# Performance work log

Hardware: AMD Instinct MI355X
Metric: run time of the kernel (lower is better)

The kernel has to match this reference:

```python
import jax, jax.numpy as jnp
import numpy as np

B, Q, S, D, H = 4, 1024, 4096, 256, 8
HD = D // H
NEG = -1000000000.0


def setup_inputs() -> dict:
    key = jax.random.key(0)
    ks = jax.random.split(key, 12)
    s = 1.0 / np.sqrt(D)
    inp = {
        "query": jax.random.normal(ks[0], (B, Q, D), jnp.float32),
        "key": jax.random.normal(ks[1], (B, S, D), jnp.float32),
        "value": jax.random.normal(ks[2], (B, S, D), jnp.float32),
        "attention_mask": jax.random.randint(ks[3], (B, Q, S), 0, 2) > 0,
        # nn.Linear weights stored as [out, in]; we apply x @ W.T + b
        "wq": jax.random.uniform(ks[4], (D, D), jnp.float32, -s, s),
        "bq": jnp.zeros((D,), jnp.float32),
        "wk": jax.random.uniform(ks[5], (D, D), jnp.float32, -s, s),
        "bk": jnp.zeros((D,), jnp.float32),
        "wv": jax.random.uniform(ks[6], (D, D), jnp.float32, -s, s),
        "bv": jnp.zeros((D,), jnp.float32),
        "wo": jax.random.uniform(ks[7], (D, D), jnp.float32, -s, s),
        "bo": jnp.zeros((D,), jnp.float32),
        "ln_g": jnp.ones((D,), jnp.float32),
        "ln_b": jnp.zeros((D,), jnp.float32),
    }
    return inp


def _layernorm(x, g, b, eps=1e-5):
    mu = jnp.mean(x, axis=-1, keepdims=True)
    var = jnp.var(x, axis=-1, keepdims=True)
    return (x - mu) * jax.lax.rsqrt(var + eps) * g + b


def reference(query, key, value, attention_mask, wq, bq, wk, bk, wv, bv, wo, bo, ln_g, ln_b):
    residual = query
    x = _layernorm(query, ln_g, ln_b)
    q = x @ wq.T + bq                       # [B,Q,D]
    k = key @ wk.T + bk                     # [B,S,D]
    v = value @ wv.T + bv                   # [B,S,D]
    q = q.reshape(B, Q, H, HD).transpose(0, 2, 1, 3)   # [B,H,Q,HD]
    k = k.reshape(B, S, H, HD).transpose(0, 2, 1, 3)   # [B,H,S,HD]
    v = v.reshape(B, S, H, HD).transpose(0, 2, 1, 3)   # [B,H,S,HD]
    scale = HD ** -0.5
    scores = jnp.einsum("bhqd,bhsd->bhqs", q, k) * scale   # [B,H,Q,S]
    scores = jnp.where(attention_mask[:, None, :, :], scores, NEG)
    attn = jax.nn.softmax(scores, axis=-1)
    # dropout is identity in eval/inference mode
    out = jnp.einsum("bhqs,bhsd->bhqd", attn, v)            # [B,H,Q,HD]
    out = out.transpose(0, 2, 1, 3).reshape(B, Q, D)
    out = out @ wo.T + bo
    return out + residual
```

## Files before the change

### kernel.cpp

```cpp
#include <hip/hip_runtime.h>
#include <cmath>

#define BQ 4
#define QL 1024
#define SL 4096
#define DM 256
#define NH 8
#define HD 32
#define NROWS 32768
#define NSPLIT 4
#define SEG (SL / NSPLIT)

typedef __attribute__((ext_vector_type(8))) short short8;
typedef __attribute__((ext_vector_type(4))) short short4v;
typedef __attribute__((ext_vector_type(4))) float f32x4;
typedef __attribute__((ext_vector_type(4))) unsigned int uint4v;
typedef unsigned long long u64;

#define MFMA16(a, b, c) __builtin_amdgcn_mfma_f32_16x16x32_bf16((a), (b), (c), 0, 0, 0)

__device__ __forceinline__ short f2bf(float f) {
  union { float f; unsigned int u; } x; x.f = f;
  unsigned int r = x.u + 0x7FFFu + ((x.u >> 16) & 1u);
  return (short)(r >> 16);
}
__device__ __forceinline__ unsigned int fu(float f) {
  union { float f; unsigned int u; } x; x.f = f; return x.u;
}

__global__ __launch_bounds__(256) void wcvt_kernel(const float* __restrict__ wq,
                                                   const float* __restrict__ wk,
                                                   const float* __restrict__ wv,
                                                   const float* __restrict__ wo,
                                                   const uint4v* __restrict__ mask4,
                                                   unsigned int* __restrict__ flags,
                                                   short* __restrict__ w16) {
  if (blockIdx.x == 0) {
    __shared__ int fA, fB;
    if (threadIdx.x == 0) { fA = 0; fB = 0; }
    __syncthreads();
    unsigned int a = 0, bb = 0;
#pragma unroll
    for (int i = 0; i < 16; ++i) {
      uint4v v = mask4[threadIdx.x * 16 + i];
#pragma unroll
      for (int e = 0; e < 4; ++e) {
        a |= (v[e] & 0xFEFEFEFEu);
        bb |= (v[e] & 0xFFFFFF00u);
      }
    }
    if (a) atomicOr(&fA, 1);
    if (bb) atomicOr(&fB, 1);
    __syncthreads();
    if (threadIdx.x == 0) flags[0] = (fA || !fB) ? 4u : 1u;
  }
  const int i = blockIdx.x * 256 + threadIdx.x;
  const float* src;
  short* dst;
  if (i < 8192)       { src = wq + i * 8;            dst = w16 + i * 8; }
  else if (i < 16384) { src = wk + (i - 8192) * 8;   dst = w16 + 65536 + (i - 8192) * 8; }
  else if (i < 24576) { src = wv + (i - 16384) * 8;  dst = w16 + 131072 + (i - 16384) * 8; }
  else                { src = wo + (i - 24576) * 8;  dst = w16 + 196608 + (i - 24576) * 8; }
  f32x4 a0 = *(const f32x4*)src;
  f32x4 a1 = *(const f32x4*)(src + 4);
  short8 o;
#pragma unroll
  for (int e = 0; e < 4; ++e) { o[e] = f2bf(a0[e]); o[4 + e] = f2bf(a1[e]); }
  *(short8*)dst = o;
}

__global__ __launch_bounds__(256) void maskbits_kernel(const void* __restrict__ mask,
                                                       const unsigned int* __restrict__ flags,
                                                       u64* __restrict__ MB) {
  const int i = blockIdx.x * 256 + threadIdx.x;
  u64 bits = 0;
  if (flags[0] == 4u) {
    const uint4v* src = (const uint4v*)mask + (size_t)i * 16;
#pragma unroll
    for (int c = 0; c < 16; ++c) {
      uint4v v = src[c];
      unsigned int nib = 0;
#pragma unroll
      for (int e = 0; e < 4; ++e) nib |= (v[e] != 0u ? 1u : 0u) << e;
      bits |= (u64)nib << ((c & 3) * 16 + (c >> 2) * 4);
    }
  } else {
    const uint4v* src = (const uint4v*)mask + (size_t)i * 4;
#pragma unroll
    for (int c = 0; c < 4; ++c) {
      uint4v v = src[c];
#pragma unroll
      for (int e4 = 0; e4 < 4; ++e4) {
        const unsigned int u = v[e4];
        unsigned int nib = 0;
        nib |= (u & 0x000000FFu) ? 1u : 0u;
        nib |= (u & 0x0000FF00u) ? 2u : 0u;
        nib |= (u & 0x00FF0000u) ? 4u : 0u;
        nib |= (u & 0xFF000000u) ? 8u : 0u;
        bits |= (u64)nib << (e4 * 16 + c * 4);
      }
    }
  }
  MB[i] = bits;
}

__global__ __launch_bounds__(256) void ln_q_kernel(const float* __restrict__ x,
                                                   const float* __restrict__ gw,
                                                   const float* __restrict__ bw,
                                                   short* __restrict__ out) {
  const int lane = threadIdx.x & 63;
  const int row = blockIdx.x * 4 + (threadIdx.x >> 6);
  const float* xr = x + (size_t)row * DM;
  f32x4 v = *(const f32x4*)(xr + lane * 4);
  float s = v[0] + v[1] + v[2] + v[3];
  float s2 = v[0]*v[0] + v[1]*v[1] + v[2]*v[2] + v[3]*v[3];
#pragma unroll
  for (int m = 1; m < 64; m <<= 1) { s += __shfl_xor(s, m); s2 += __shfl_xor(s2, m); }
  const float mu = s * (1.0f / DM);
  const float var = s2 * (1.0f / DM) - mu * mu;
  const float inv = rsqrtf(var + 1e-5f);
  f32x4 gv = *(const f32x4*)(gw + lane * 4);
  f32x4 bv = *(const f32x4*)(bw + lane * 4);
  short4v o;
#pragma unroll
  for (int i = 0; i < 4; ++i) o[i] = f2bf((v[i] - mu) * inv * gv[i] + bv[i]);
  *(short4v*)(out + (size_t)row * DM + lane * 4) = o;
}

template <int AF32, int EPI>
__global__ __launch_bounds__(256) void gemm_bt(const void* __restrict__ Ap,
                                               const short* __restrict__ W16,
                                               const float* __restrict__ bias,
                                               void* __restrict__ outp,
                                               const float* __restrict__ resid,
                                               float oscale) {
  __shared__ __align__(16) short As[64][72];
  __shared__ __align__(16) short Bs[64][72];
  const int t = threadIdx.x;
  const int lane = t & 63, w = t >> 6;
  const int wm = w >> 1, wn = w & 1;
  const int g = lane >> 4, lr = lane & 15, gsh = g * 4;
  const int bid = blockIdx.x;
  const int x = bid & 7, j = bid >> 3;
  const int mt8 = gridDim.x >> 5;
  const int m0 = (x * mt8 + (j >> 2)) * 64;
  const int n0 = (j & 3) * 64;
  const int row = (t * 2) >> 3, cc0 = (t * 2) & 7;
  f32x4 acc[2][2] = {};

  const float* Af = (const float*)Ap;
  const short* A16 = (const short*)Ap;
  f32x4 apf[2][2];
  short8 aps[2];
  short8 bn[2];
#pragma unroll
  for (int c = 0; c < 2; ++c) {
    if (AF32) {
      const float* s = Af + (size_t)(m0 + row) * DM + (cc0 + c) * 8;
      apf[c][0] = *(const f32x4*)s;
      apf[c][1] = *(const f32x4*)(s + 4);
    } else {
      aps[c] = *(const short8*)(A16 + (size_t)(m0 + row) * DM + (cc0 + c) * 8);
    }
    bn[c] = *(const short8*)(W16 + (size_t)(n0 + row) * DM + (cc0 + c) * 8);
  }
  for (int k0 = 0; k0 < DM; k0 += 64) {
    if (k0) __syncthreads();
#pragma unroll
    for (int c = 0; c < 2; ++c) {
      short8 sv;
      if (AF32) {
#pragma unroll
        for (int e = 0; e < 4; ++e) { sv[e] = f2bf(apf[c][0][e]); sv[4 + e] = f2bf(apf[c][1][e]); }
      } else {
        sv = aps[c];
      }
      *(short8*)&As[row][(cc0 + c) * 8] = sv;
      *(short8*)&Bs[row][(cc0 + c) * 8] = bn[c];
    }
    __syncthreads();
    if (k0 < DM - 64) {
#pragma unroll
      for (int c = 0; c < 2; ++c) {
        if (AF32) {
          const float* s = Af + (size_t)(m0 + row) * DM + k0 + 64 + (cc0 + c) * 8;
          apf[c][0] = *(const f32x4*)s;
          apf[c][1] = *(const f32x4*)(s + 4);
        } else {
          aps[c] = *(const short8*)(A16 + (size_t)(m0 + row) * DM + k0 + 64 + (cc0 + c) * 8);
        }
        bn[c] = *(const short8*)(W16 + (size_t)(n0 + row) * DM + k0 + 64 + (cc0 + c) * 8);
      }
    }
#pragma unroll
    for (int ks = 0; ks < 2; ++ks) {
      short8 af[2], bfr[2];
#pragma unroll
      for (int i = 0; i < 2; ++i) af[i] = *(const short8*)&As[wm * 32 + i * 16 + lr][ks * 32 + g * 8];
#pragma unroll
      for (int jj = 0; jj < 2; ++jj) bfr[jj] = *(const short8*)&Bs[wn * 32 + jj * 16 + lr][ks * 32 + g * 8];
#pragma unroll
      for (int i = 0; i < 2; ++i)
#pragma unroll
        for (int jj = 0; jj < 2; ++jj) acc[i][jj] = MFMA16(af[i], bfr[jj], acc[i][jj]);
    }
  }
  if (EPI == 2) {
#pragma unroll
    for (int i = 0; i < 2; ++i)
#pragma unroll
      for (int jj = 0; jj < 2; ++jj)
#pragma unroll
        for (int r = 0; r < 4; ++r) {
          const int rr = m0 + wm * 32 + i * 16 + gsh + r;
          const int col = n0 + wn * 32 + jj * 16 + lr;
          ((float*)outp)[(size_t)rr * DM + col] =
              acc[i][jj][r] + bias[col] + resid[(size_t)rr * DM + col];
        }
  } else if (EPI == 0 || EPI == 1) {
    __syncthreads();
#pragma unroll
    for (int i = 0; i < 2; ++i)
#pragma unroll
      for (int jj = 0; jj < 2; ++jj) {
        const int nl = wn * 32 + jj * 16 + lr;
        const float bv = bias[n0 + nl];
#pragma unroll
        for (int r = 0; r < 4; ++r)
          As[wm * 32 + i * 16 + gsh + r][nl] = f2bf((acc[i][jj][r] + bv) * oscale);
      }
    __syncthreads();
#pragma unroll
    for (int c = 0; c < 2; ++c) {
      const int idx = t * 2 + c, dl = idx >> 3, ch = idx & 7;
      *(short8*)((short*)outp + (size_t)(m0 + dl) * DM + n0 + ch * 8) =
          *(const short8*)&As[dl][ch * 8];
    }
  } else {
    __syncthreads();
#pragma unroll
    for (int i = 0; i < 2; ++i)
#pragma unroll
      for (int jj = 0; jj < 2; ++jj) {
        const int nl = wn * 32 + jj * 16 + lr;
        const float bv = bias[n0 + nl];
        short4v pk4;
#pragma unroll
        for (int r = 0; r < 4; ++r) pk4[r] = f2bf(acc[i][jj][r] + bv);
        *(short4v*)&As[nl][wm * 32 + i * 16 + gsh] = pk4;
      }
    __syncthreads();
    const int bidx = m0 >> 12, sbase = m0 & (SL - 1);
#pragma unroll
    for (int c = 0; c < 2; ++c) {
      const int idx = t * 2 + c, dl = idx >> 3, ch = idx & 7;
      *(short8*)((short*)outp + ((size_t)bidx * DM + n0 + dl) * SL + sbase + ch * 8) =
          *(const short8*)&As[dl][ch * 8];
    }
  }
}

__global__ __launch_bounds__(256, 4) void attn_kernel(const short* __restrict__ qb,
                                                      const short* __restrict__ kb,
                                                      const short* __restrict__ vbT,
                                                      const unsigned short* __restrict__ MB,
                                                      float* __restrict__ Op,
                                                      float* __restrict__ Lp) {
  __shared__ __align__(16) short Ks[2][64][40];
  __shared__ __align__(16) short Vs[2][32][76];

  const int n_ = blockIdx.x;
  const int x_ = n_ & 7, j_ = n_ >> 3;
  const int grp = ((j_ >> 5) << 3) + x_;
  const int within = j_ & 31;
  const int q0 = (within & 7) * 128;
  const int split = within >> 3;
  const int h = grp & 7, b = grp >> 3;

  const int t = threadIdx.x;
  const int l = t & 63, w = t >> 6;
  const int g = l >> 4, lr = l & 15, gsh = g * 4;
  const int qbase = q0 + w * 32;
  const int srow = t >> 2, scc = t & 3;
  const int vd = t >> 3, vsc = t & 7;

  const short* Kp = kb + ((size_t)b * SL + split * SEG + srow) * DM + h * HD + scc * 8;
  const short* Vp = vbT + ((size_t)(b * NH + h) * HD + vd) * SL + split * SEG + vsc * 8;
  const unsigned short* MBp0 =
      MB + (((size_t)(b * QL) + qbase + lr) * 64 + split * (SEG / 64)) * 4 + g;
  const unsigned short* MBp1 = MBp0 + 16 * 64 * 4;

  const short8 qf0 =
      *(const short8*)(qb + ((size_t)(b * QL) + qbase + lr) * DM + h * HD + g * 8);
  const short8 qf1 =
      *(const short8*)(qb + ((size_t)(b * QL) + qbase + 16 + lr) * DM + h * HD + g * 8);

  const short ONE = (short)0x3F80;
  const short8 ONES = {ONE, ONE, ONE, ONE, ONE, ONE, ONE, ONE};
  f32x4 Ov0[2] = {}, Ov1[2] = {};
  f32x4 Ls0 = {0.f, 0.f, 0.f, 0.f}, Ls1 = {0.f, 0.f, 0.f, 0.f};

  short8 kreg[2], vreg[2];
  unsigned int mbA[2], mbB[2];
  kreg[0] = *(const short8*)Kp;
  vreg[0] = *(const short8*)Vp;
  mbA[0] = MBp0[0]; mbB[0] = MBp1[0];
  kreg[1] = *(const short8*)(Kp + (size_t)64 * DM);
  vreg[1] = *(const short8*)(Vp + 64);
  mbA[1] = MBp0[4]; mbB[1] = MBp1[4];

#pragma unroll 2
  for (int it = 0; it < SEG / 64; ++it) {
    const int buf = it & 1;
    *(short8*)&Ks[buf][srow][scc * 8] = kreg[buf];
    {
      short4v lo = {vreg[buf][0], vreg[buf][1], vreg[buf][2], vreg[buf][3]};
      short4v hi = {vreg[buf][4], vreg[buf][5], vreg[buf][6], vreg[buf][7]};
      *(short4v*)&Vs[buf][vd][vsc * 8] = lo;
      *(short4v*)&Vs[buf][vd][vsc * 8 + 4] = hi;
    }
    const unsigned int mb0 = mbA[buf], mb1 = mbB[buf];
    __syncthreads();
    if (it < SEG / 64 - 2) {
      kreg[buf] = *(const short8*)(Kp + (size_t)(it + 2) * 64 * DM);
      vreg[buf] = *(const short8*)(Vp + (it + 2) * 64);
      mbA[buf] = MBp0[(it + 2) * 4];
      mbB[buf] = MBp1[(it + 2) * 4];
    }

    const f32x4 z = {0.f, 0.f, 0.f, 0.f};
    f32x4 sc0[4], sc1[4];
#pragma unroll
    for (int f = 0; f < 4; ++f) {
      short8 kf = *(const short8*)&Ks[buf][f * 16 + lr][g * 8];
      sc0[f] = MFMA16(kf, qf0, z);
      sc1[f] = MFMA16(kf, qf1, z);
    }
#pragma unroll
    for (int ks = 0; ks < 2; ++ks) {
      unsigned int pk0[2][2], pk1[2][2];
#pragma unroll
      for (int fi = 0; fi < 2; ++fi) {
        const int f = 2 * ks + fi;
        unsigned int p0[4], p1[4];
#pragma unroll
        for (int r = 0; r < 4; ++r) {
          const unsigned int m0b = (unsigned int)(-(int)((mb0 >> (f * 4 + r)) & 1u));
          const unsigned int m1b = (unsigned int)(-(int)((mb1 >> (f * 4 + r)) & 1u));
          p0[r] = fu(__builtin_amdgcn_exp2f(sc0[f][r])) & m0b;
          p1[r] = fu(__builtin_amdgcn_exp2f(sc1[f][r])) & m1b;
        }
        pk0[fi][0] = __builtin_amdgcn_perm(p0[0], p0[1], 0x03020706u);
        pk0[fi][1] = __builtin_amdgcn_perm(p0[2], p0[3], 0x03020706u);
        pk1[fi][0] = __builtin_amdgcn_perm(p1[0], p1[1], 0x03020706u);
        pk1[fi][1] = __builtin_amdgcn_perm(p1[2], p1[3], 0x03020706u);
      }
      union { unsigned int u[4]; short8 v; } pa0, pa1;
      pa0.u[0] = pk0[0][0]; pa0.u[1] = pk0[0][1]; pa0.u[2] = pk0[1][0]; pa0.u[3] = pk0[1][1];
      pa1.u[0] = pk1[0][0]; pa1.u[1] = pk1[0][1]; pa1.u[2] = pk1[1][0]; pa1.u[3] = pk1[1][1];
      Ls0 = MFMA16(pa0.v, ONES, Ls0);
      Ls1 = MFMA16(pa1.v, ONES, Ls1);
#pragma unroll
      for (int n = 0; n < 2; ++n) {
        short4v va = *(const short4v*)&Vs[buf][n * 16 + lr][(2 * ks) * 16 + gsh];
        short4v vb2 = *(const short4v*)&Vs[buf][n * 16 + lr][(2 * ks + 1) * 16 + gsh];
        union { short4v h[2]; short8 v; } vf;
        vf.h[0] = va; vf.h[1] = vb2;
        Ov0[n] = MFMA16(pa0.v, vf.v, Ov0[n]);
        Ov1[n] = MFMA16(pa1.v, vf.v, Ov1[n]);
      }
    }
  }
  const int ridx = (b * NH + h) * QL + qbase;
  const size_t pb = (size_t)split * NROWS + ridx;
#pragma unroll
  for (int n = 0; n < 2; ++n)
#pragma unroll
    for (int r = 0; r < 4; ++r) {
      Op[(pb + gsh + r) * 32 + n * 16 + lr] = Ov0[n][r];
      Op[(pb + 16 + gsh + r) * 32 + n * 16 + lr] = Ov1[n][r];
    }
  if (lr == 0) {
#pragma unroll
    for (int r = 0; r < 4; ++r) {
      Lp[pb + gsh + r] = Ls0[r];
      Lp[pb + 16 + gsh + r] = Ls1[r];
    }
  }
}

__global__ __launch_bounds__(256) void combine_kernel(const float* __restrict__ Op,
                                                      const float* __restrict__ Lp,
                                                      short* __restrict__ ao) {
  const int tid = blockIdx.x * 256 + threadIdx.x;
  const int r = tid >> 3;
  const int dq = (tid & 7) * 4;
  float den = 0.0f;
  f32x4 acc = {0.f, 0.f, 0.f, 0.f};
#pragma unroll
  for (int i = 0; i < NSPLIT; ++i) {
    den += Lp[(size_t)i * NROWS + r];
    const f32x4 o = *(const f32x4*)(Op + ((size_t)i * NROWS + r) * 32 + dq);
#pragma unroll
    for (int e = 0; e < 4; ++e) acc[e] += o[e];
  }
  const float inv = __builtin_amdgcn_rcpf(den);
  const int b = r >> 13, h = (r >> 10) & 7, q = r & 1023;
  short4v o;
#pragma unroll
  for (int i = 0; i < 4; ++i) o[i] = f2bf(acc[i] * inv);
  *(short4v*)(ao + ((size_t)(b * QL + q)) * DM + h * HD + dq) = o;
}

extern "C" void kernel_launch(void* const* d_in, const int* in_sizes, int n_in,
                              void* d_out, int out_size, void* d_ws, size_t ws_size,
                              hipStream_t stream) {
  const float* query = (const float*)d_in[0];
  const float* key   = (const float*)d_in[1];
  const float* value = (const float*)d_in[2];
  const void*  mask  = d_in[3];
  const float* wq = (const float*)d_in[4];
  const float* bq = (const float*)d_in[5];
  const float* wk = (const float*)d_in[6];
  const float* bk = (const float*)d_in[7];
  const float* wv = (const float*)d_in[8];
  const float* bv = (const float*)d_in[9];
  const float* wo = (const float*)d_in[10];
  const float* bo = (const float*)d_in[11];
  const float* lng = (const float*)d_in[12];
  const float* lnb = (const float*)d_in[13];
  float* out = (float*)d_out;

  char* ws = (char*)d_ws;
  unsigned int* flags = (unsigned int*)ws;
  float* Lp  = (float*)(ws + (4u << 10));
  short* xln = (short*)(ws + (2u << 20));
  short* qb  = (short*)(ws + (4u << 20));
  short* kb  = (short*)(ws + (6u << 20));
  short* vbT = (short*)(ws + (14u << 20));
  u64*   mbt = (u64*)(ws + (22u << 20));
  short* w16 = (short*)(ws + (24u << 20));
  float* Op  = (float*)(ws + (25u << 20));
  short* ao  = (short*)(ws + (41u << 20));

  const float qscale = (float)(1.4426950408889634 / sqrt((double)HD));

  wcvt_kernel<<<128, 256, 0, stream>>>(wq, wk, wv, wo, (const uint4v*)mask, flags, w16);
  maskbits_kernel<<<1024, 256, 0, stream>>>(mask, flags, mbt);
  ln_q_kernel<<<(BQ * QL) / 4, 256, 0, stream>>>(query, lng, lnb, xln);
  gemm_bt<0, 0><<<(BQ * QL / 64) * 4, 256, 0, stream>>>(xln, w16, bq, qb, nullptr, qscale);
  gemm_bt<1, 1><<<(BQ * SL / 64) * 4, 256, 0, stream>>>(key, w16 + 65536, bk, kb, nullptr, 1.0f);
  gemm_bt<1, 3><<<(BQ * SL / 64) * 4, 256, 0, stream>>>(value, w16 + 131072, bv, vbT, nullptr, 1.0f);
  attn_kernel<<<1024, 256, 0, stream>>>(qb, kb, vbT, (const unsigned short*)mbt, Op, Lp);
  combine_kernel<<<1024, 256, 0, stream>>>(Op, Lp, ao);
  gemm_bt<0, 2><<<(BQ * QL / 64) * 4, 256, 0, stream>>>(ao, w16 + 196608, bo, out, query, 1.0f);
}
```

Baseline: 94.83 us.

## Halve attention query tile per block to double grid and occupancy

Each attention block now processes 64 query rows (16 per wave) instead of 128 (32 per wave), and the grid grows from 1024 to 2048 blocks with launch bounds raised to 8 blocks per CU. The aim is more waves in flight to hide memory and MFMA latency. In exchange, every K/V tile is loaded from global memory and staged through LDS twice as often, which lowers reuse per loaded byte.

After: 110.9 us. 16.9% more time.

```diff
diff --git a/kernel.cpp b/kernel.cpp
--- a/kernel.cpp
+++ b/kernel.cpp
@@ -260,7 +260,7 @@
   }
 }
 
-__global__ __launch_bounds__(256, 4) void attn_kernel(const short* __restrict__ qb,
+__global__ __launch_bounds__(256, 8) void attn_kernel(const short* __restrict__ qb,
                                                       const short* __restrict__ kb,
                                                       const short* __restrict__ vbT,
                                                       const unsigned short* __restrict__ MB,
@@ -271,43 +271,40 @@
 
   const int n_ = blockIdx.x;
   const int x_ = n_ & 7, j_ = n_ >> 3;
-  const int grp = ((j_ >> 5) << 3) + x_;
-  const int within = j_ & 31;
-  const int q0 = (within & 7) * 128;
-  const int split = within >> 3;
+  const int grp = ((j_ >> 6) << 3) + x_;
+  const int within = j_ & 63;
+  const int q0 = (within & 15) * 64;
+  const int split = within >> 4;
   const int h = grp & 7, b = grp >> 3;
 
   const int t = threadIdx.x;
   const int l = t & 63, w = t >> 6;
   const int g = l >> 4, lr = l & 15, gsh = g * 4;
-  const int qbase = q0 + w * 32;
+  const int qbase = q0 + w * 16;
   const int srow = t >> 2, scc = t & 3;
   const int vd = t >> 3, vsc = t & 7;
 
   const short* Kp = kb + ((size_t)b * SL + split * SEG + srow) * DM + h * HD + scc * 8;
   const short* Vp = vbT + ((size_t)(b * NH + h) * HD + vd) * SL + split * SEG + vsc * 8;
-  const unsigned short* MBp0 =
+  const unsigned short* MBp =
       MB + (((size_t)(b * QL) + qbase + lr) * 64 + split * (SEG / 64)) * 4 + g;
-  const unsigned short* MBp1 = MBp0 + 16 * 64 * 4;
-
-  const short8 qf0 =
+
+  const short8 qf =
       *(const short8*)(qb + ((size_t)(b * QL) + qbase + lr) * DM + h * HD + g * 8);
-  const short8 qf1 =
-      *(const short8*)(qb + ((size_t)(b * QL) + qbase + 16 + lr) * DM + h * HD + g * 8);
 
   const short ONE = (short)0x3F80;
   const short8 ONES = {ONE, ONE, ONE, ONE, ONE, ONE, ONE, ONE};
-  f32x4 Ov0[2] = {}, Ov1[2] = {};
-  f32x4 Ls0 = {0.f, 0.f, 0.f, 0.f}, Ls1 = {0.f, 0.f, 0.f, 0.f};
+  f32x4 Ov[2] = {};
+  f32x4 Ls = {0.f, 0.f, 0.f, 0.f};
 
   short8 kreg[2], vreg[2];
-  unsigned int mbA[2], mbB[2];
+  unsigned int mbA[2];
   kreg[0] = *(const short8*)Kp;
   vreg[0] = *(const short8*)Vp;
-  mbA[0] = MBp0[0]; mbB[0] = MBp1[0];
+  mbA[0] = MBp[0];
   kreg[1] = *(const short8*)(Kp + (size_t)64 * DM);
   vreg[1] = *(const short8*)(Vp + 64);
-  mbA[1] = MBp0[4]; mbB[1] = MBp1[4];
+  mbA[1] = MBp[4];
 
 #pragma unroll 2
   for (int it = 0; it < SEG / 64; ++it) {
@@ -319,55 +316,46 @@
       *(short4v*)&Vs[buf][vd][vsc * 8] = lo;
       *(short4v*)&Vs[buf][vd][vsc * 8 + 4] = hi;
     }
-    const unsigned int mb0 = mbA[buf], mb1 = mbB[buf];
+    const unsigned int mb = mbA[buf];
     __syncthreads();
     if (it < SEG / 64 - 2) {
       kreg[buf] = *(const short8*)(Kp + (size_t)(it + 2) * 64 * DM);
       vreg[buf] = *(const short8*)(Vp + (it + 2) * 64);
-      mbA[buf] = MBp0[(it + 2) * 4];
-      mbB[buf] = MBp1[(it + 2) * 4];
+      mbA[buf] = MBp[(it + 2) * 4];
     }
 
     const f32x4 z = {0.f, 0.f, 0.f, 0.f};
-    f32x4 sc0[4], sc1[4];
+    f32x4 sc[4];
 #pragma unroll
     for (int f = 0; f < 4; ++f) {
       short8 kf = *(const short8*)&Ks[buf][f * 16 + lr][g * 8];
-      sc0[f] = MFMA16(kf, qf0, z);
-      sc1[f] = MFMA16(kf, qf1, z);
+      sc[f] = MFMA16(kf, qf, z);
     }
 #pragma unroll
     for (int ks = 0; ks < 2; ++ks) {
-      unsigned int pk0[2][2], pk1[2][2];
+      unsigned int pk[2][2];
 #pragma unroll
       for (int fi = 0; fi < 2; ++fi) {
         const int f = 2 * ks + fi;
-        unsigned int p0[4], p1[4];
+        unsigned int p[4];
 #pragma unroll
         for (int r = 0; r < 4; ++r) {
-          const unsigned int m0b = (unsigned int)(-(int)((mb0 >> (f * 4 + r)) & 1u));
-          const unsigned int m1b = (unsigned int)(-(int)((mb1 >> (f * 4 + r)) & 1u));
-          p0[r] = fu(__builtin_amdgcn_exp2f(sc0[f][r])) & m0b;
-          p1[r] = fu(__builtin_amdgcn_exp2f(sc1[f][r])) & m1b;
+          const unsigned int mbit = (unsigned int)(-(int)((mb >> (f * 4 + r)) & 1u));
+          p[r] = fu(__builtin_amdgcn_exp2f(sc[f][r])) & mbit;
         }
-        pk0[fi][0] = __builtin_amdgcn_perm(p0[0], p0[1], 0x03020706u);
-        pk0[fi][1] = __builtin_amdgcn_perm(p0[2], p0[3], 0x03020706u);
-        pk1[fi][0] = __builtin_amdgcn_perm(p1[0], p1[1], 0x03020706u);
-        pk1[fi][1] = __builtin_amdgcn_perm(p1[2], p1[3], 0x03020706u);
-      }
-      union { unsigned int u[4]; short8 v; } pa0, pa1;
-      pa0.u[0] = pk0[0][0]; pa0.u[1] = pk0[0][1]; pa0.u[2] = pk0[1][0]; pa0.u[3] = pk0[1][1];
-      pa1.u[0] = pk1[0][0]; pa1.u[1] = pk1[0][1]; pa1.u[2] = pk1[1][0]; pa1.u[3] = pk1[1][1];
-      Ls0 = MFMA16(pa0.v, ONES, Ls0);
-      Ls1 = MFMA16(pa1.v, ONES, Ls1);
+        pk[fi][0] = __builtin_amdgcn_perm(p[0], p[1], 0x03020706u);
+        pk[fi][1] = __builtin_amdgcn_perm(p[2], p[3], 0x03020706u);
+      }
+      union { unsigned int u[4]; short8 v; } pa;
+      pa.u[0] = pk[0][0]; pa.u[1] = pk[0][1]; pa.u[2] = pk[1][0]; pa.u[3] = pk[1][1];
+      Ls = MFMA16(pa.v, ONES, Ls);
 #pragma unroll
       for (int n = 0; n < 2; ++n) {
         short4v va = *(const short4v*)&Vs[buf][n * 16 + lr][(2 * ks) * 16 + gsh];
         short4v vb2 = *(const short4v*)&Vs[buf][n * 16 + lr][(2 * ks + 1) * 16 + gsh];
         union { short4v h[2]; short8 v; } vf;
         vf.h[0] = va; vf.h[1] = vb2;
-        Ov0[n] = MFMA16(pa0.v, vf.v, Ov0[n]);
-        Ov1[n] = MFMA16(pa1.v, vf.v, Ov1[n]);
+        Ov[n] = MFMA16(pa.v, vf.v, Ov[n]);
       }
     }
   }
@@ -376,16 +364,11 @@
 #pragma unroll
   for (int n = 0; n < 2; ++n)
 #pragma unroll
-    for (int r = 0; r < 4; ++r) {
-      Op[(pb + gsh + r) * 32 + n * 16 + lr] = Ov0[n][r];
-      Op[(pb + 16 + gsh + r) * 32 + n * 16 + lr] = Ov1[n][r];
-    }
+    for (int r = 0; r < 4; ++r)
+      Op[(pb + gsh + r) * 32 + n * 16 + lr] = Ov[n][r];
   if (lr == 0) {
 #pragma unroll
-    for (int r = 0; r < 4; ++r) {
-      Lp[pb + gsh + r] = Ls0[r];
-      Lp[pb + 16 + gsh + r] = Ls1[r];
-    }
+    for (int r = 0; r < 4; ++r) Lp[pb + gsh + r] = Ls[r];
   }
 }
 
@@ -451,7 +434,7 @@
   gemm_bt<0, 0><<<(BQ * QL / 64) * 4, 256, 0, stream>>>(xln, w16, bq, qb, nullptr, qscale);
   gemm_bt<1, 1><<<(BQ * SL / 64) * 4, 256, 0, stream>>>(key, w16 + 65536, bk, kb, nullptr, 1.0f);
   gemm_bt<1, 3><<<(BQ * SL / 64) * 4, 256, 0, stream>>>(value, w16 + 131072, bv, vbT, nullptr, 1.0f);
-  attn_kernel<<<1024, 256, 0, stream>>>(qb, kb, vbT, (const unsigned short*)mbt, Op, Lp);
+  attn_kernel<<<2048, 256, 0, stream>>>(qb, kb, vbT, (const unsigned short*)mbt, Op, Lp);
   combine_kernel<<<1024, 256, 0, stream>>>(Op, Lp, ao);
   gemm_bt<0, 2><<<(BQ * QL / 64) * 4, 256, 0, stream>>>(ao, w16 + 196608, bo, out, query, 1.0f);
 }
```
